# Optimization experiments

Hardware: AMD Instinct MI355X
Metric: run time of the kernel (lower is better)

The kernel has to match this reference:

```python
import jax, jax.numpy as jnp
import numpy as np

N_VERTS = 100000
N_JOINTS = 24
N_BETAS = 10
N_POSEDIRS = 207  # (24-1)*9
# Standard SMPL kinematic tree parents
PARENTS = np.array([-1, 0, 0, 0, 1, 2, 3, 4, 5, 6, 7, 8, 9, 9, 9, 12, 13, 14, 16, 17, 18, 19, 20, 21])


def setup_inputs() -> dict:
    key = jax.random.key(0)
    ks = jax.random.split(key, 9)
    f = jnp.float32
    return {
        "betas": jax.random.normal(ks[0], (N_BETAS,), f),
        "pose": jax.random.normal(ks[1], (N_JOINTS, 3), f) * 0.2,
        "scale": jnp.ones((1,), f),
        "trans": jax.random.normal(ks[2], (3,), f),
        "v_template": jax.random.normal(ks[3], (N_VERTS, 3), f),
        "shapedirs": jax.random.normal(ks[4], (N_VERTS, 3, N_BETAS), f) * 0.01,
        "posedirs": jax.random.normal(ks[5], (N_VERTS, 3, N_POSEDIRS), f) * 0.01,
        "J_regressor": jax.random.uniform(ks[6], (N_JOINTS, N_VERTS), f) / N_VERTS,
        "weights": jax.nn.softmax(jax.random.normal(ks[7], (N_VERTS, N_JOINTS), f), axis=-1),
    }


def rodrigues(r):
    """Axis-angle [J,3] -> rotation matrices [J,3,3] (matches torch impl; eps kept tiny+deterministic)."""
    theta = jnp.linalg.norm(r + 1e-8, axis=-1, keepdims=True)  # [J,1]
    r_hat = r / theta
    z = jnp.zeros_like(r_hat[:, 0])
    K = jnp.stack([z, -r_hat[:, 2], r_hat[:, 1],
                   r_hat[:, 2], z, -r_hat[:, 0],
                   -r_hat[:, 1], r_hat[:, 0], z], axis=1).reshape(-1, 3, 3)
    c = jnp.cos(theta)[..., None]  # [J,1,1]
    s = jnp.sin(theta)[..., None]
    outer = r_hat[:, :, None] * r_hat[:, None, :]  # [J,3,3]
    I = jnp.eye(3, dtype=r.dtype)
    return c * I + (1.0 - c) * outer + s * K


def reference(betas, pose, scale, trans, v_template, shapedirs, posedirs, J_regressor, weights):
    dt = v_template.dtype
    # blend shapes
    v_shaped = jnp.einsum('vks,s->vk', shapedirs, betas) + v_template  # [V,3]
    J = J_regressor @ v_shaped  # [24,3]
    R = rodrigues(pose)  # [24,3,3]
    I3 = jnp.eye(3, dtype=dt)
    lrotmin = (R[1:] - I3).reshape(-1)  # [207]
    v_posed = v_shaped + jnp.einsum('vkp,p->vk', posedirs, lrotmin)  # [V,3]
    # forward kinematics over 24-joint chain
    bottom = jnp.array([[0.0, 0.0, 0.0, 1.0]], dtype=dt)
    def make_A(Ri, t):
        return jnp.concatenate([jnp.concatenate([Ri, t[:, None]], axis=1), bottom], axis=0)  # [4,4]
    As = [make_A(R[0], J[0])]
    for i in range(1, N_JOINTS):
        p = int(PARENTS[i])
        As.append(As[p] @ make_A(R[i], J[i] - J[p]))
    G = jnp.stack(As)  # [24,4,4]
    # remove rest-pose joint locations
    Jh = jnp.concatenate([J, jnp.zeros((N_JOINTS, 1), dt)], axis=1)  # [24,4]
    corr = jnp.einsum('jab,jb->ja', G, Jh)  # [24,4]
    rel = G - jnp.concatenate([jnp.zeros((N_JOINTS, 4, 3), dt), corr[:, :, None]], axis=2)
    # linear blend skinning
    T = jnp.einsum('vj,jab->vab', weights, rel)  # [V,4,4]
    vh = jnp.concatenate([v_posed, jnp.ones((v_posed.shape[0], 1), dt)], axis=1)  # [V,4]
    v = jnp.einsum('vab,vb->va', T, vh)[:, :3]  # [V,3]
    return v * scale.reshape(()) + trans[None, :]
```

## Files before the change

### kernel.cpp

```cpp
#include <hip/hip_runtime.h>

#define NV 100000
#define NJ 24
#define NP 207
#define NPART 25
#define VPB 8
#define NTILES (NV / VPB)
#define TF4 1242
#define GRIDF 1024

__global__ __launch_bounds__(256) void k_shape(
    const float* __restrict__ betas, const float* __restrict__ v_template,
    const float* __restrict__ shapedirs, float* __restrict__ v_shaped) {
  __shared__ float sb[10];
  if (threadIdx.x < 10) sb[threadIdx.x] = betas[threadIdx.x];
  __syncthreads();
  int R = blockIdx.x * 256 + threadIdx.x;
  if (R >= 3 * NV) return;
  const float2* sd = (const float2*)(shapedirs + (size_t)R * 10);
  float a = v_template[R];
  #pragma unroll
  for (int s = 0; s < 5; ++s) {
    float2 x = sd[s];
    a += x.x * sb[2 * s] + x.y * sb[2 * s + 1];
  }
  v_shaped[R] = a;
}

__global__ __launch_bounds__(256) void k_jreg(
    const float* __restrict__ Jreg, const float* __restrict__ v_shaped,
    float* __restrict__ jpart) {
  int j = blockIdx.x, part = blockIdx.y, tid = threadIdx.x;
  const int SL = NV / NPART;
  int v0 = part * SL;
  const float4* w4 = (const float4*)(Jreg + (size_t)j * NV + v0);
  const float4* s4 = (const float4*)(v_shaped + (size_t)3 * v0);
  float s0 = 0.f, s1 = 0.f, s2 = 0.f;
  for (int i4 = tid; i4 < SL / 4; i4 += 256) {
    float4 w = w4[i4];
    float4 A = s4[3 * i4 + 0];
    float4 B = s4[3 * i4 + 1];
    float4 C = s4[3 * i4 + 2];
    s0 += w.x * A.x + w.y * A.w + w.z * B.z + w.w * C.y;
    s1 += w.x * A.y + w.y * B.x + w.z * B.w + w.w * C.z;
    s2 += w.x * A.z + w.y * B.y + w.z * C.x + w.w * C.w;
  }
  __shared__ float red[256][3];
  red[tid][0] = s0; red[tid][1] = s1; red[tid][2] = s2;
  __syncthreads();
  for (int off = 128; off > 0; off >>= 1) {
    if (tid < off) {
      red[tid][0] += red[tid + off][0];
      red[tid][1] += red[tid + off][1];
      red[tid][2] += red[tid + off][2];
    }
    __syncthreads();
  }
  if (tid < 3) jpart[(part * NJ + j) * 3 + tid] = red[0][tid];
}

__global__ __launch_bounds__(64) void k_fk(
    const float* __restrict__ pose, const float* __restrict__ jpart,
    float* __restrict__ lrot, float* __restrict__ rel) {
  __shared__ float J[NJ][3];
  __shared__ float R[NJ][9];
  __shared__ float G[NJ][12];
  int tid = threadIdx.x;
  if (tid < NJ) {
    for (int k = 0; k < 3; ++k) {
      float a = 0.f;
      for (int part = 0; part < NPART; ++part) a += jpart[(part * NJ + tid) * 3 + k];
      J[tid][k] = a;
    }
    float rx = pose[tid * 3 + 0], ry = pose[tid * 3 + 1], rz = pose[tid * 3 + 2];
    float tx = rx + 1e-8f, ty = ry + 1e-8f, tz = rz + 1e-8f;
    float theta = sqrtf(tx * tx + ty * ty + tz * tz);
    float x = rx / theta, y = ry / theta, z = rz / theta;
    float c = cosf(theta), s = sinf(theta), C = 1.f - c;
    float* Rr = R[tid];
    Rr[0] = c + C * x * x;     Rr[1] = C * x * y - s * z; Rr[2] = C * x * z + s * y;
    Rr[3] = C * x * y + s * z; Rr[4] = c + C * y * y;     Rr[5] = C * y * z - s * x;
    Rr[6] = C * x * z - s * y; Rr[7] = C * y * z + s * x; Rr[8] = c + C * z * z;
    if (tid >= 1) {
      #pragma unroll
      for (int e = 0; e < 9; ++e) {
        float id = (e == 0 || e == 4 || e == 8) ? 1.f : 0.f;
        lrot[(tid - 1) * 9 + e] = Rr[e] - id;
      }
    }
  }
  __syncthreads();
  if (tid == 0) {
    const int par[NJ] = {-1,0,0,0,1,2,3,4,5,6,7,8,9,9,9,12,13,14,16,17,18,19,20,21};
    for (int a = 0; a < 3; ++a) {
      for (int b = 0; b < 3; ++b) G[0][a * 4 + b] = R[0][a * 3 + b];
      G[0][a * 4 + 3] = J[0][a];
    }
    for (int i = 1; i < NJ; ++i) {
      int p = par[i];
      float t0 = J[i][0] - J[p][0], t1 = J[i][1] - J[p][1], t2 = J[i][2] - J[p][2];
      for (int a = 0; a < 3; ++a) {
        float g0 = G[p][a * 4 + 0], g1 = G[p][a * 4 + 1], g2 = G[p][a * 4 + 2];
        for (int b = 0; b < 3; ++b)
          G[i][a * 4 + b] = g0 * R[i][0 * 3 + b] + g1 * R[i][1 * 3 + b] + g2 * R[i][2 * 3 + b];
        G[i][a * 4 + 3] = G[p][a * 4 + 3] + g0 * t0 + g1 * t1 + g2 * t2;
      }
    }
  }
  __syncthreads();
  if (tid < NJ) {
    for (int a = 0; a < 3; ++a) {
      float corr = G[tid][a * 4 + 0] * J[tid][0] + G[tid][a * 4 + 1] * J[tid][1] +
                   G[tid][a * 4 + 2] * J[tid][2];
      rel[tid * 12 + a * 4 + 0] = G[tid][a * 4 + 0];
      rel[tid * 12 + a * 4 + 1] = G[tid][a * 4 + 1];
      rel[tid * 12 + a * 4 + 2] = G[tid][a * 4 + 2];
      rel[tid * 12 + a * 4 + 3] = G[tid][a * 4 + 3] - corr;
    }
  }
}

__device__ __forceinline__ void stage_tile(float4* dst, const float4* src, int tid) {
  #pragma unroll
  for (int r = 0; r < 5; ++r) {
    int i4 = r * 256 + tid;
    if (i4 < TF4) {
      __builtin_amdgcn_global_load_lds(
          (const __attribute__((address_space(1))) void*)(src + i4),
          (__attribute__((address_space(3))) void*)(dst + r * 256 + (tid & 192)),
          16, 0, 0);
    }
  }
}

__global__ __launch_bounds__(256, 4) void k_fused(
    const float* __restrict__ posedirs, const float* __restrict__ weights,
    const float* __restrict__ lrot, const float* __restrict__ rel,
    const float* __restrict__ scale, const float* __restrict__ trans,
    float* __restrict__ vbuf) {
  __shared__ float4 tile[2][TF4];
  int tid = threadIdx.x;
  int wid = tid >> 6, lane = tid & 63, half = lane >> 5, lj = lane & 31;

  int t0 = blockIdx.x;
  const float4* pd4 = (const float4*)posedirs;
  stage_tile(&tile[0][0], pd4 + (size_t)t0 * TF4, tid);

  float llr[7];
  #pragma unroll
  for (int e = 0; e < 7; ++e) {
    int p = lj + 32 * e;
    llr[e] = (p < NP) ? lrot[p] : 0.f;
  }
  float rlq[12];
  #pragma unroll
  for (int e = 0; e < 12; ++e) rlq[e] = (lj < NJ) ? rel[lj * 12 + e] : 0.f;
  float sc = scale[0];
  float tr = (lj < 3) ? trans[lj] : 0.f;

  int nt = (NTILES - 1 - t0) / GRIDF + 1;
  __syncthreads();

  for (int it = 0; it < nt; ++it) {
    int cur = it & 1;
    int tcur = t0 + it * GRIDF;
    int vv = tcur * VPB + (wid << 1) + half;
    float wj = (lj < NJ) ? weights[(size_t)vv * NJ + lj] : 0.f;
    int tnext = t0 + (it + 1) * GRIDF;
    if (tnext >= NTILES) tnext = NTILES - 1;
    stage_tile(&tile[cur ^ 1][0], pd4 + (size_t)tnext * TF4, tid);
    asm volatile("s_waitcnt vmcnt(5)" ::: "memory");
    __builtin_amdgcn_sched_barrier(0);
    __builtin_amdgcn_s_barrier();
    __builtin_amdgcn_sched_barrier(0);

    float pvl = (lj < 3) ? vbuf[(size_t)3 * vv + lj] : 0.f;

    const float* row = (const float*)&tile[cur][0] + ((wid << 1) + half) * (3 * NP);
    float a0 = 0.f, a1 = 0.f, a2 = 0.f;
    #pragma unroll
    for (int e = 0; e < 7; ++e) {
      int p = lj + 32 * e;
      if (p < NP) {
        float l = llr[e];
        a0 += row[p] * l;
        a1 += row[NP + p] * l;
        a2 += row[2 * NP + p] * l;
      }
    }
    #pragma unroll
    for (int off = 16; off > 0; off >>= 1) {
      a0 += __shfl_xor(a0, off);
      a1 += __shfl_xor(a1, off);
      a2 += __shfl_xor(a2, off);
    }
    int gb = lane & 32;
    float p0 = __shfl(pvl, gb + 0) + a0;
    float p1 = __shfl(pvl, gb + 1) + a1;
    float p2 = __shfl(pvl, gb + 2) + a2;
    float q0 = rlq[0] * p0 + rlq[1] * p1 + rlq[2]  * p2 + rlq[3];
    float q1 = rlq[4] * p0 + rlq[5] * p1 + rlq[6]  * p2 + rlq[7];
    float q2 = rlq[8] * p0 + rlq[9] * p1 + rlq[10] * p2 + rlq[11];
    float r0 = wj * q0, r1 = wj * q1, r2 = wj * q2;
    #pragma unroll
    for (int off = 16; off > 0; off >>= 1) {
      r0 += __shfl_xor(r0, off);
      r1 += __shfl_xor(r1, off);
      r2 += __shfl_xor(r2, off);
    }
    if (lj < 3) {
      float oo = (lj == 0) ? r0 : (lj == 1) ? r1 : r2;
      vbuf[(size_t)3 * vv + lj] = oo * sc + tr;
    }
    __builtin_amdgcn_sched_barrier(0);
    __builtin_amdgcn_s_barrier();
    __builtin_amdgcn_sched_barrier(0);
  }
  asm volatile("s_waitcnt vmcnt(0)" ::: "memory");
}

extern "C" void kernel_launch(void* const* d_in, const int* in_sizes, int n_in,
                              void* d_out, int out_size, void* d_ws, size_t ws_size,
                              hipStream_t stream) {
  const float* betas      = (const float*)d_in[0];
  const float* pose       = (const float*)d_in[1];
  const float* scale      = (const float*)d_in[2];
  const float* trans      = (const float*)d_in[3];
  const float* v_template = (const float*)d_in[4];
  const float* shapedirs  = (const float*)d_in[5];
  const float* posedirs   = (const float*)d_in[6];
  const float* Jreg       = (const float*)d_in[7];
  const float* weights    = (const float*)d_in[8];
  float* out = (float*)d_out;
  float* ws  = (float*)d_ws;

  float* jpart = ws;
  float* lrot  = ws + 1800;
  float* rel   = ws + 2048;

  k_shape<<<(3 * NV + 255) / 256, 256, 0, stream>>>(betas, v_template, shapedirs, out);
  k_jreg<<<dim3(NJ, NPART), 256, 0, stream>>>(Jreg, out, jpart);
  k_fk<<<1, 64, 0, stream>>>(pose, jpart, lrot, rel);
  k_fused<<<GRIDF, 256, 0, stream>>>(posedirs, weights, lrot, rel, scale, trans, out);
}
```

Baseline: 68.27 us.

## Fuse shape blend with joint regression and give fused kernel contiguous tile ranges

Merges the shape-blend and joint-regressor kernels into one, where each block computes a slice of v_shaped in shared memory and immediately reduces it against J_regressor, writing transposed per-block partials that the FK kernel sums with vector loads. This removes one launch and the re-read of v_shaped from global memory. The skinning kernel now assigns each block a contiguous run of tiles instead of a grid stride, and hoists the vbuf load ahead of the barrier. The fused partial layout adds a 250-way reduction in the single-block FK kernel, and the fused kernel's 250 blocks may give lower parallelism than the previous split.

```diff
diff --git a/kernel.cpp b/kernel.cpp
--- a/kernel.cpp
+++ b/kernel.cpp
@@ -3,75 +3,87 @@
 #define NV 100000
 #define NJ 24
 #define NP 207
-#define NPART 25
 #define VPB 8
 #define NTILES (NV / VPB)
 #define TF4 1242
 #define GRIDF 1024
-
-__global__ __launch_bounds__(256) void k_shape(
+#define SJBLK 250
+#define VSLICE 400
+
+__global__ __launch_bounds__(256) void k_sj(
     const float* __restrict__ betas, const float* __restrict__ v_template,
-    const float* __restrict__ shapedirs, float* __restrict__ v_shaped) {
+    const float* __restrict__ shapedirs, const float* __restrict__ Jreg,
+    float* __restrict__ vbuf, float* __restrict__ jpartT) {
   __shared__ float sb[10];
-  if (threadIdx.x < 10) sb[threadIdx.x] = betas[threadIdx.x];
-  __syncthreads();
-  int R = blockIdx.x * 256 + threadIdx.x;
-  if (R >= 3 * NV) return;
-  const float2* sd = (const float2*)(shapedirs + (size_t)R * 10);
-  float a = v_template[R];
-  #pragma unroll
-  for (int s = 0; s < 5; ++s) {
-    float2 x = sd[s];
-    a += x.x * sb[2 * s] + x.y * sb[2 * s + 1];
-  }
-  v_shaped[R] = a;
-}
-
-__global__ __launch_bounds__(256) void k_jreg(
-    const float* __restrict__ Jreg, const float* __restrict__ v_shaped,
-    float* __restrict__ jpart) {
-  int j = blockIdx.x, part = blockIdx.y, tid = threadIdx.x;
-  const int SL = NV / NPART;
-  int v0 = part * SL;
-  const float4* w4 = (const float4*)(Jreg + (size_t)j * NV + v0);
-  const float4* s4 = (const float4*)(v_shaped + (size_t)3 * v0);
-  float s0 = 0.f, s1 = 0.f, s2 = 0.f;
-  for (int i4 = tid; i4 < SL / 4; i4 += 256) {
-    float4 w = w4[i4];
-    float4 A = s4[3 * i4 + 0];
-    float4 B = s4[3 * i4 + 1];
-    float4 C = s4[3 * i4 + 2];
-    s0 += w.x * A.x + w.y * A.w + w.z * B.z + w.w * C.y;
-    s1 += w.x * A.y + w.y * B.x + w.z * B.w + w.w * C.z;
-    s2 += w.x * A.z + w.y * B.y + w.z * C.x + w.w * C.w;
-  }
-  __shared__ float red[256][3];
-  red[tid][0] = s0; red[tid][1] = s1; red[tid][2] = s2;
-  __syncthreads();
-  for (int off = 128; off > 0; off >>= 1) {
-    if (tid < off) {
-      red[tid][0] += red[tid + off][0];
-      red[tid][1] += red[tid + off][1];
-      red[tid][2] += red[tid + off][2];
-    }
-    __syncthreads();
-  }
-  if (tid < 3) jpart[(part * NJ + j) * 3 + tid] = red[0][tid];
-}
-
-__global__ __launch_bounds__(64) void k_fk(
-    const float* __restrict__ pose, const float* __restrict__ jpart,
+  __shared__ float vsh[VSLICE * 3];
+  int tid = threadIdx.x, bb = blockIdx.x;
+  int w = tid >> 6, lane = tid & 63;
+  if (tid < 10) sb[tid] = betas[tid];
+  __syncthreads();
+  int R0 = bb * (VSLICE * 3);
+  for (int r = tid; r < VSLICE * 3; r += 256) {
+    int Rg = R0 + r;
+    const float2* sd = (const float2*)(shapedirs + (size_t)Rg * 10);
+    float a = v_template[Rg];
+    #pragma unroll
+    for (int s = 0; s < 5; ++s) {
+      float2 x = sd[s];
+      a += x.x * sb[2 * s] + x.y * sb[2 * s + 1];
+    }
+    vsh[r] = a;
+    vbuf[Rg] = a;
+  }
+  __syncthreads();
+  int v0 = bb * VSLICE;
+  #pragma unroll
+  for (int jj = 0; jj < 6; ++jj) {
+    int j = 6 * w + jj;
+    float s0 = 0.f, s1 = 0.f, s2 = 0.f;
+    #pragma unroll
+    for (int i = 0; i < 7; ++i) {
+      int vo = lane + 64 * i;
+      if (vo < VSLICE) {
+        float wv = Jreg[(size_t)j * NV + v0 + vo];
+        s0 += wv * vsh[3 * vo + 0];
+        s1 += wv * vsh[3 * vo + 1];
+        s2 += wv * vsh[3 * vo + 2];
+      }
+    }
+    #pragma unroll
+    for (int off = 32; off > 0; off >>= 1) {
+      s0 += __shfl_xor(s0, off);
+      s1 += __shfl_xor(s1, off);
+      s2 += __shfl_xor(s2, off);
+    }
+    if (lane == 0) {
+      jpartT[(j * 3 + 0) * 256 + bb] = s0;
+      jpartT[(j * 3 + 1) * 256 + bb] = s1;
+      jpartT[(j * 3 + 2) * 256 + bb] = s2;
+    }
+  }
+}
+
+__global__ __launch_bounds__(128) void k_fk(
+    const float* __restrict__ pose, const float* __restrict__ jpartT,
     float* __restrict__ lrot, float* __restrict__ rel) {
-  __shared__ float J[NJ][3];
+  __shared__ float J[NJ * 3];
   __shared__ float R[NJ][9];
   __shared__ float G[NJ][12];
   int tid = threadIdx.x;
+  if (tid < NJ * 3) {
+    const float4* p4 = (const float4*)(jpartT + tid * 256);
+    float a = 0.f;
+    #pragma unroll 8
+    for (int i = 0; i < SJBLK / 4; ++i) {
+      float4 x = p4[i];
+      a += x.x + x.y + x.z + x.w;
+    }
+    #pragma unroll
+    for (int i = (SJBLK / 4) * 4; i < SJBLK; ++i) a += jpartT[tid * 256 + i];
+    J[tid] = a;
+  }
+  __syncthreads();
   if (tid < NJ) {
-    for (int k = 0; k < 3; ++k) {
-      float a = 0.f;
-      for (int part = 0; part < NPART; ++part) a += jpart[(part * NJ + tid) * 3 + k];
-      J[tid][k] = a;
-    }
     float rx = pose[tid * 3 + 0], ry = pose[tid * 3 + 1], rz = pose[tid * 3 + 2];
     float tx = rx + 1e-8f, ty = ry + 1e-8f, tz = rz + 1e-8f;
     float theta = sqrtf(tx * tx + ty * ty + tz * tz);
@@ -94,11 +106,13 @@
     const int par[NJ] = {-1,0,0,0,1,2,3,4,5,6,7,8,9,9,9,12,13,14,16,17,18,19,20,21};
     for (int a = 0; a < 3; ++a) {
       for (int b = 0; b < 3; ++b) G[0][a * 4 + b] = R[0][a * 3 + b];
-      G[0][a * 4 + 3] = J[0][a];
+      G[0][a * 4 + 3] = J[a];
     }
     for (int i = 1; i < NJ; ++i) {
       int p = par[i];
-      float t0 = J[i][0] - J[p][0], t1 = J[i][1] - J[p][1], t2 = J[i][2] - J[p][2];
+      float t0 = J[i * 3 + 0] - J[p * 3 + 0];
+      float t1 = J[i * 3 + 1] - J[p * 3 + 1];
+      float t2 = J[i * 3 + 2] - J[p * 3 + 2];
       for (int a = 0; a < 3; ++a) {
         float g0 = G[p][a * 4 + 0], g1 = G[p][a * 4 + 1], g2 = G[p][a * 4 + 2];
         for (int b = 0; b < 3; ++b)
@@ -110,8 +124,9 @@
   __syncthreads();
   if (tid < NJ) {
     for (int a = 0; a < 3; ++a) {
-      float corr = G[tid][a * 4 + 0] * J[tid][0] + G[tid][a * 4 + 1] * J[tid][1] +
-                   G[tid][a * 4 + 2] * J[tid][2];
+      float corr = G[tid][a * 4 + 0] * J[tid * 3 + 0] +
+                   G[tid][a * 4 + 1] * J[tid * 3 + 1] +
+                   G[tid][a * 4 + 2] * J[tid * 3 + 2];
       rel[tid * 12 + a * 4 + 0] = G[tid][a * 4 + 0];
       rel[tid * 12 + a * 4 + 1] = G[tid][a * 4 + 1];
       rel[tid * 12 + a * 4 + 2] = G[tid][a * 4 + 2];
@@ -139,12 +154,14 @@
     const float* __restrict__ scale, const float* __restrict__ trans,
     float* __restrict__ vbuf) {
   __shared__ float4 tile[2][TF4];
-  int tid = threadIdx.x;
+  int tid = threadIdx.x, b = blockIdx.x;
   int wid = tid >> 6, lane = tid & 63, half = lane >> 5, lj = lane & 31;
 
-  int t0 = blockIdx.x;
+  int s_b = b * 12 + (b < 212 ? b : 212);
+  int nt = 12 + (b < 212 ? 1 : 0);
+
   const float4* pd4 = (const float4*)posedirs;
-  stage_tile(&tile[0][0], pd4 + (size_t)t0 * TF4, tid);
+  stage_tile(&tile[0][0], pd4 + (size_t)s_b * TF4, tid);
 
   float llr[7];
   #pragma unroll
@@ -158,23 +175,20 @@
   float sc = scale[0];
   float tr = (lj < 3) ? trans[lj] : 0.f;
 
-  int nt = (NTILES - 1 - t0) / GRIDF + 1;
   __syncthreads();
 
   for (int it = 0; it < nt; ++it) {
     int cur = it & 1;
-    int tcur = t0 + it * GRIDF;
-    int vv = tcur * VPB + (wid << 1) + half;
+    int vv = (s_b + it) * VPB + (wid << 1) + half;
+    float pvl = (lj < 3) ? vbuf[(size_t)3 * vv + lj] : 0.f;
     float wj = (lj < NJ) ? weights[(size_t)vv * NJ + lj] : 0.f;
-    int tnext = t0 + (it + 1) * GRIDF;
+    int tnext = s_b + it + 1;
     if (tnext >= NTILES) tnext = NTILES - 1;
     stage_tile(&tile[cur ^ 1][0], pd4 + (size_t)tnext * TF4, tid);
     asm volatile("s_waitcnt vmcnt(5)" ::: "memory");
     __builtin_amdgcn_sched_barrier(0);
     __builtin_amdgcn_s_barrier();
     __builtin_amdgcn_sched_barrier(0);
-
-    float pvl = (lj < 3) ? vbuf[(size_t)3 * vv + lj] : 0.f;
 
     const float* row = (const float*)&tile[cur][0] + ((wid << 1) + half) * (3 * NP);
     float a0 = 0.f, a1 = 0.f, a2 = 0.f;
@@ -234,12 +248,11 @@
   float* out = (float*)d_out;
   float* ws  = (float*)d_ws;
 
-  float* jpart = ws;
-  float* lrot  = ws + 1800;
-  float* rel   = ws + 2048;
-
-  k_shape<<<(3 * NV + 255) / 256, 256, 0, stream>>>(betas, v_template, shapedirs, out);
-  k_jreg<<<dim3(NJ, NPART), 256, 0, stream>>>(Jreg, out, jpart);
-  k_fk<<<1, 64, 0, stream>>>(pose, jpart, lrot, rel);
+  float* jpartT = ws;
+  float* lrot   = ws + 18432;
+  float* rel    = ws + 18688;
+
+  k_sj<<<SJBLK, 256, 0, stream>>>(betas, v_template, shapedirs, Jreg, out, jpartT);
+  k_fk<<<1, 128, 0, stream>>>(pose, jpartT, lrot, rel);
   k_fused<<<GRIDF, 256, 0, stream>>>(posedirs, weights, lrot, rel, scale, trans, out);
 }
```

Measured after the change: 73.30 us. 1.07x slower.

## Triple-buffer posedirs tiles and prefetch per-vertex inputs one iteration ahead

Applied to the files above, without the earlier changes.

The fused skinning kernel goes from double to triple LDS buffering, so posedirs tiles are staged two iterations ahead instead of one. The per-vertex v_shaped and weights loads are also issued one iteration early, so their latency overlaps with the current tile's compute. To fit three 20 KB tiles, the grid is halved to 512 blocks and the occupancy hint drops to 2 blocks per CU. That leaves fewer resident waves to hide latency, and the fixed vmcnt(10) wait is conservative.

```diff
diff --git a/kernel.cpp b/kernel.cpp
--- a/kernel.cpp
+++ b/kernel.cpp
@@ -7,7 +7,7 @@
 #define VPB 8
 #define NTILES (NV / VPB)
 #define TF4 1242
-#define GRIDF 1024
+#define GRIDF 512
 
 __global__ __launch_bounds__(256) void k_shape(
     const float* __restrict__ betas, const float* __restrict__ v_template,
@@ -133,18 +133,22 @@
   }
 }
 
-__global__ __launch_bounds__(256, 4) void k_fused(
-    const float* __restrict__ posedirs, const float* __restrict__ weights,
+__global__ __launch_bounds__(256, 2) void k_fused(
+    const float* __restrict__ posedirs, const float* __restrict__ wgt,
     const float* __restrict__ lrot, const float* __restrict__ rel,
     const float* __restrict__ scale, const float* __restrict__ trans,
     float* __restrict__ vbuf) {
-  __shared__ float4 tile[2][TF4];
-  int tid = threadIdx.x;
+  __shared__ float4 tile[3][TF4];
+  int tid = threadIdx.x, b = blockIdx.x;
   int wid = tid >> 6, lane = tid & 63, half = lane >> 5, lj = lane & 31;
-
-  int t0 = blockIdx.x;
   const float4* pd4 = (const float4*)posedirs;
-  stage_tile(&tile[0][0], pd4 + (size_t)t0 * TF4, tid);
+
+  int vv0 = b * VPB + (wid << 1) + half;
+  float pvl = (lj < 3) ? vbuf[(size_t)3 * vv0 + lj] : 0.f;
+  float wj  = (lj < NJ) ? wgt[(size_t)vv0 * NJ + lj] : 0.f;
+  __builtin_amdgcn_sched_barrier(0);
+  stage_tile(&tile[0][0], pd4 + (size_t)b * TF4, tid);
+  stage_tile(&tile[1][0], pd4 + (size_t)(b + GRIDF) * TF4, tid);
 
   float llr[7];
   #pragma unroll
@@ -158,25 +162,28 @@
   float sc = scale[0];
   float tr = (lj < 3) ? trans[lj] : 0.f;
 
-  int nt = (NTILES - 1 - t0) / GRIDF + 1;
-  __syncthreads();
+  float4* bc = &tile[0][0];
+  float4* bn = &tile[1][0];
+  float4* bs = &tile[2][0];
+  int nt = (NTILES - 1 - b) / GRIDF + 1;
 
   for (int it = 0; it < nt; ++it) {
-    int cur = it & 1;
-    int tcur = t0 + it * GRIDF;
-    int vv = tcur * VPB + (wid << 1) + half;
-    float wj = (lj < NJ) ? weights[(size_t)vv * NJ + lj] : 0.f;
-    int tnext = t0 + (it + 1) * GRIDF;
-    if (tnext >= NTILES) tnext = NTILES - 1;
-    stage_tile(&tile[cur ^ 1][0], pd4 + (size_t)tnext * TF4, tid);
-    asm volatile("s_waitcnt vmcnt(5)" ::: "memory");
+    int tnE = b + (it + 1) * GRIDF;
+    if (tnE >= NTILES) tnE = NTILES - 1;
+    int vvn = tnE * VPB + (wid << 1) + half;
+    float pvl_n = (lj < 3) ? vbuf[(size_t)3 * vvn + lj] : 0.f;
+    float wj_n  = (lj < NJ) ? wgt[(size_t)vvn * NJ + lj] : 0.f;
+    __builtin_amdgcn_sched_barrier(0);
+    int tst = b + (it + 2) * GRIDF;
+    if (tst >= NTILES) tst = NTILES - 1;
+    stage_tile(bs, pd4 + (size_t)tst * TF4, tid);
+    asm volatile("s_waitcnt vmcnt(10)" ::: "memory");
     __builtin_amdgcn_sched_barrier(0);
     __builtin_amdgcn_s_barrier();
     __builtin_amdgcn_sched_barrier(0);
 
-    float pvl = (lj < 3) ? vbuf[(size_t)3 * vv + lj] : 0.f;
-
-    const float* row = (const float*)&tile[cur][0] + ((wid << 1) + half) * (3 * NP);
+    int vv = (b + it * GRIDF) * VPB + (wid << 1) + half;
+    const float* row = (const float*)bc + ((wid << 1) + half) * (3 * NP);
     float a0 = 0.f, a1 = 0.f, a2 = 0.f;
     #pragma unroll
     for (int e = 0; e < 7; ++e) {
@@ -215,6 +222,9 @@
     __builtin_amdgcn_sched_barrier(0);
     __builtin_amdgcn_s_barrier();
     __builtin_amdgcn_sched_barrier(0);
+
+    pvl = pvl_n; wj = wj_n;
+    float4* tmp = bc; bc = bn; bn = bs; bs = tmp;
   }
   asm volatile("s_waitcnt vmcnt(0)" ::: "memory");
 }
```

Result: slower. 70.95 us (+3.9%).
